# Kernel optimization log

Measured on AMD Instinct MI355X. Metric: run time of the kernel, lower is better.

The kernel has to match this reference:

```python
import jax, jax.numpy as jnp
import numpy as np

N = 50000
IN_CH = 128
HID = 64
HEADS = 4
OUT_CH = 2
E = 800000
NEG_SLOPE = 0.2


def setup_inputs() -> dict:
    key = jax.random.key(0)
    ks = jax.random.split(key, 10)
    x = jax.random.normal(ks[0], (N, IN_CH), dtype=jnp.float32)
    edge_index = jax.random.randint(ks[1], (2, E), 0, N, dtype=jnp.int64)
    # layer 1: GATConv(IN_CH -> HID, heads=HEADS, concat=True)
    s1 = 1.0 / np.sqrt(IN_CH)
    W1 = jax.random.normal(ks[2], (IN_CH, HEADS * HID), dtype=jnp.float32) * s1
    a_src1 = jax.random.normal(ks[3], (HEADS, HID), dtype=jnp.float32) * (1.0 / np.sqrt(HID))
    a_dst1 = jax.random.normal(ks[4], (HEADS, HID), dtype=jnp.float32) * (1.0 / np.sqrt(HID))
    b1 = jnp.zeros((HEADS * HID,), dtype=jnp.float32)
    # layer 2: GATConv(HEADS*HID -> OUT_CH, heads=1, concat=False)
    s2 = 1.0 / np.sqrt(HEADS * HID)
    W2 = jax.random.normal(ks[5], (HEADS * HID, OUT_CH), dtype=jnp.float32) * s2
    a_src2 = jax.random.normal(ks[6], (1, OUT_CH), dtype=jnp.float32) * (1.0 / np.sqrt(OUT_CH))
    a_dst2 = jax.random.normal(ks[7], (1, OUT_CH), dtype=jnp.float32) * (1.0 / np.sqrt(OUT_CH))
    b2 = jnp.zeros((OUT_CH,), dtype=jnp.float32)
    return {"x": x, "edge_index": edge_index, "W1": W1, "a_src1": a_src1,
            "a_dst1": a_dst1, "b1": b1, "W2": W2, "a_src2": a_src2,
            "a_dst2": a_dst2, "b2": b2}


def gat_conv(x, W, a_src, a_dst, bias, src, dst, heads, ch, concat):
    n = x.shape[0]
    h = (x @ W).reshape(n, heads, ch)                       # [N,H,C]
    al_s = jnp.sum(h * a_src[None], axis=-1)                # [N,H]
    al_d = jnp.sum(h * a_dst[None], axis=-1)                # [N,H]
    e = al_s[src] + al_d[dst]                               # [E,H]
    e = jnp.where(e > 0, e, NEG_SLOPE * e)                  # leaky_relu
    # segment softmax over edges grouped by destination node
    m = jax.ops.segment_max(e, dst, num_segments=n)         # [N,H]
    m = jnp.where(jnp.isfinite(m), m, 0.0)
    p = jnp.exp(e - m[dst])                                 # [E,H]
    denom = jax.ops.segment_sum(p, dst, num_segments=n)     # [N,H]
    alpha = p / (denom[dst] + 1e-16)                        # [E,H]
    msg = h[src] * alpha[:, :, None]                        # [E,H,C]
    out = jax.ops.segment_sum(msg, dst, num_segments=n)     # [N,H,C]
    if concat:
        out = out.reshape(n, heads * ch) + bias
    else:
        out = out.mean(axis=1) + bias
    return out


def reference(x, edge_index, W1, a_src1, a_dst1, b1, W2, a_src2, a_dst2, b2):
    n = x.shape[0]
    # PyG GATConv default: add self-loops
    loops = jnp.arange(n, dtype=edge_index.dtype)
    src = jnp.concatenate([edge_index[0], loops])
    dst = jnp.concatenate([edge_index[1], loops])
    h = gat_conv(x, W1, a_src1, a_dst1, b1, src, dst, HEADS, HID, True)
    h = jax.nn.relu(h)
    out = gat_conv(h, W2, a_src2, a_dst2, b2, src, dst, 1, OUT_CH, False)
    return out
```

## Files before the change

kernel.cpp:

```cpp
#include <hip/hip_runtime.h>

#define NNODE 50000
#define NEDGE 800000
#define NTOT  (NEDGE + NNODE)
#define NB_SCAN 49
#define NGEMM 1564

typedef __attribute__((ext_vector_type(8))) short bf16x8;
typedef __attribute__((ext_vector_type(4))) float f32x4;
union U4B8 { uint4 u; bf16x8 b; };

__device__ __forceinline__ unsigned short f2bf(float f) {
  union { float f; unsigned u; } v; v.f = f;
  unsigned r = v.u + 0x7FFFu + ((v.u >> 16) & 1u);
  return (unsigned short)(r >> 16);
}
__device__ __forceinline__ float bflo(unsigned u) {
  union { unsigned u; float f; } v; v.u = u << 16; return v.f;
}
__device__ __forceinline__ float bfhi(unsigned u) {
  union { unsigned u; float f; } v; v.u = u & 0xFFFF0000u; return v.f;
}
__device__ __forceinline__ unsigned packbf(float a, float b) {
  return (unsigned)f2bf(a) | ((unsigned)f2bf(b) << 16);
}

__global__ __launch_bounds__(256) void k_prep(const float* __restrict__ W1,
                                              unsigned short* __restrict__ W1bT,
                                              int* __restrict__ deg) {
  const int b = (int)blockIdx.x;
  if (b < 32) {
    int flat = b * 256 + threadIdx.x;
    int k = flat >> 6, c4 = (flat & 63) << 2;
    float4 v = *(const float4*)(W1 + k * 256 + c4);
    W1bT[(c4 + 0) * 128 + k] = f2bf(v.x);
    W1bT[(c4 + 1) * 128 + k] = f2bf(v.y);
    W1bT[(c4 + 2) * 128 + k] = f2bf(v.z);
    W1bT[(c4 + 3) * 128 + k] = f2bf(v.w);
  } else {
    int i = (b - 32) * 256 + threadIdx.x;
    if (i < NNODE) deg[i] = 0;
  }
}

__global__ __launch_bounds__(256) void k_gemm_deg(
    const float* __restrict__ x, const unsigned short* __restrict__ W1bT,
    const float* __restrict__ a_s1, const float* __restrict__ a_d1,
    unsigned short* __restrict__ h1b, float* __restrict__ als1,
    float* __restrict__ ald1, const int* __restrict__ ei,
    int* __restrict__ deg) {
  __shared__ unsigned short xs[64 * 136];
  if ((int)blockIdx.x >= NGEMM) {
    int i = ((int)blockIdx.x - NGEMM) * 256 + threadIdx.x;
    if (i < NTOT) {
      int d = (i < NEDGE) ? ei[NEDGE + i] : (i - NEDGE);
      atomicAdd(deg + d, 1);
    }
    return;
  }
  const int t = threadIdx.x;
  const int rb = (int)blockIdx.x >> 1, nhalf = (int)blockIdx.x & 1;
  const int grow0 = rb * 64;
#pragma unroll
  for (int i = 0; i < 8; ++i) {
    int f = t + i * 256;
    int row = f >> 5, c4 = (f & 31) << 2;
    int gr = grow0 + row;
    float4 v = make_float4(0.f, 0.f, 0.f, 0.f);
    if (gr < NNODE) v = *(const float4*)(x + gr * 128 + c4);
    *(uint2*)(xs + row * 136 + c4) = make_uint2(packbf(v.x, v.y), packbf(v.z, v.w));
  }
  const int wid = t >> 6, lane = t & 63;
  const int wrow = (wid >> 1) * 32;
  const int head = nhalf * 2 + (wid & 1);
  const int c_lo = lane & 15, g = lane >> 4;
  U4B8 bfr[4][4];
#pragma unroll
  for (int nr = 0; nr < 4; ++nr) {
    int c = head * 64 + nr * 16 + c_lo;
#pragma unroll
    for (int ks = 0; ks < 4; ++ks)
      bfr[nr][ks].u = *(const uint4*)(W1bT + c * 128 + ks * 32 + g * 8);
  }
  __syncthreads();
  U4B8 afr[2][4];
#pragma unroll
  for (int mr = 0; mr < 2; ++mr)
#pragma unroll
    for (int ks = 0; ks < 4; ++ks)
      afr[mr][ks].u = *(const uint4*)(xs + (wrow + mr * 16 + c_lo) * 136 + ks * 32 + g * 8);
  f32x4 acc[2][4];
#pragma unroll
  for (int mr = 0; mr < 2; ++mr)
#pragma unroll
    for (int nr = 0; nr < 4; ++nr) acc[mr][nr] = (f32x4){0.f, 0.f, 0.f, 0.f};
#pragma unroll
  for (int ks = 0; ks < 4; ++ks)
#pragma unroll
    for (int mr = 0; mr < 2; ++mr)
#pragma unroll
      for (int nr = 0; nr < 4; ++nr)
        acc[mr][nr] = __builtin_amdgcn_mfma_f32_16x16x32_bf16(
            afr[mr][ks].b, bfr[nr][ks].b, acc[mr][nr], 0, 0, 0);
  float as_v[4], ad_v[4];
#pragma unroll
  for (int nr = 0; nr < 4; ++nr) {
    as_v[nr] = a_s1[head * 64 + nr * 16 + c_lo];
    ad_v[nr] = a_d1[head * 64 + nr * 16 + c_lo];
  }
  float ps[2][4], pd[2][4];
#pragma unroll
  for (int mr = 0; mr < 2; ++mr)
#pragma unroll
    for (int r = 0; r < 4; ++r) {
      float s = 0.f, dsum = 0.f;
#pragma unroll
      for (int nr = 0; nr < 4; ++nr) {
        s += acc[mr][nr][r] * as_v[nr];
        dsum += acc[mr][nr][r] * ad_v[nr];
      }
      ps[mr][r] = s; pd[mr][r] = dsum;
    }
#pragma unroll
  for (int m = 1; m < 16; m <<= 1)
#pragma unroll
    for (int mr = 0; mr < 2; ++mr)
#pragma unroll
      for (int r = 0; r < 4; ++r) {
        ps[mr][r] += __shfl_xor(ps[mr][r], m, 64);
        pd[mr][r] += __shfl_xor(pd[mr][r], m, 64);
      }
  if (c_lo == 0) {
#pragma unroll
    for (int mr = 0; mr < 2; ++mr)
#pragma unroll
      for (int r = 0; r < 4; ++r) {
        int node = grow0 + wrow + mr * 16 + g * 4 + r;
        if (node < NNODE) {
          als1[node * 4 + head] = ps[mr][r];
          ald1[node * 4 + head] = pd[mr][r];
        }
      }
  }
  __syncthreads();
  unsigned short* tb = xs + wid * 2048;
#pragma unroll
  for (int mr = 0; mr < 2; ++mr)
#pragma unroll
    for (int nr = 0; nr < 4; ++nr)
#pragma unroll
      for (int r = 0; r < 4; ++r)
        tb[(mr * 16 + g * 4 + r) * 64 + nr * 16 + c_lo] = f2bf(acc[mr][nr][r]);
#pragma unroll
  for (int i = 0; i < 4; ++i) {
    int unit = i * 64 + lane;
    int row = unit >> 3, cS = (unit & 7) * 8;
    int node = grow0 + wrow + row;
    if (node < NNODE) {
      uint4 v = *(const uint4*)(tb + unit * 8);
      *(uint4*)(h1b + (size_t)node * 256 + nhalf * 128 + (wid & 1) * 64 + cS) = v;
    }
  }
}

__global__ __launch_bounds__(1024) void k_scan1(const int* __restrict__ deg,
                                                int* __restrict__ rowptr,
                                                int* __restrict__ bsum) {
  __shared__ int sh[1024];
  const int t = threadIdx.x;
  const int idx = (int)blockIdx.x * 1024 + t;
  int v = (idx < NNODE) ? deg[idx] : 0;
  sh[t] = v;
  __syncthreads();
#pragma unroll
  for (int off = 1; off < 1024; off <<= 1) {
    int add = (t >= off) ? sh[t - off] : 0;
    __syncthreads();
    sh[t] += add;
    __syncthreads();
  }
  if (idx < NNODE) rowptr[idx + 1] = sh[t];
  if (t == 1023) bsum[blockIdx.x] = sh[1023];
}

__global__ __launch_bounds__(256) void k_scan23(const int* __restrict__ deg,
                                                int* __restrict__ rowptr,
                                                const int* __restrict__ bsum,
                                                int* __restrict__ cursor) {
  __shared__ int boff[64];
  const int t = threadIdx.x;
  if (t < 64) {
    int v = (t < NB_SCAN) ? bsum[t] : 0;
    int orig = v;
#pragma unroll
    for (int off = 1; off < 64; off <<= 1) {
      int n = __shfl_up(v, off, 64);
      if (t >= off) v += n;
    }
    boff[t] = v - orig;
  }
  __syncthreads();
  int idx = (int)blockIdx.x * 256 + t;
  if (idx < NNODE) {
    int incl = rowptr[idx + 1] + boff[idx >> 10];
    rowptr[idx + 1] = incl;
    cursor[idx] = incl - deg[idx];
    if (idx == 0) rowptr[0] = 0;
  }
}

__global__ void k_scatter(const int* __restrict__ ei, int* __restrict__ cursor,
                          int* __restrict__ esrc) {
  int i = (int)blockIdx.x * blockDim.x + threadIdx.x;
  if (i >= NTOT) return;
  int s, d;
  if (i < NEDGE) { s = ei[i]; d = ei[NEDGE + i]; }
  else           { s = i - NEDGE; d = s; }
  int pos = atomicAdd(cursor + d, 1);
  esrc[pos] = s;
}

__global__ __launch_bounds__(256) void k_agg1(
    const unsigned short* __restrict__ h1b, const float* __restrict__ als1,
    const float* __restrict__ ald1, const int* __restrict__ rowptr,
    const int* __restrict__ esrc, const float* __restrict__ b1,
    const float* __restrict__ W2, const float* __restrict__ a_s2,
    const float* __restrict__ a_d2, float4* __restrict__ h2c) {
  const int w = threadIdx.x >> 6, lane = threadIdx.x & 63;
  const int d = (int)blockIdx.x * 4 + w;
  const int half = lane >> 5, cl = lane & 31;
  const int head = cl >> 3;
  const float ald = ald1[d * 4 + head];
  const int begin = rowptr[d], end = rowptr[d + 1];
  float acc[8];
#pragma unroll
  for (int i = 0; i < 8; ++i) acc[i] = 0.f;
  float S = 0.f;

  int j = begin + half;
  int s = (j < end) ? esrc[j] : -1;
  while (s >= 0) {
    const uint4 hv = *(const uint4*)(h1b + (size_t)s * 256 + cl * 8);
    float e = als1[s * 4 + head] + ald;
    int jn = j + 2;
    int sn = (jn < end) ? esrc[jn] : -1;
    e = fmaxf(e, 0.2f * e);
    float wgt = __expf(e);
    S += wgt;
    acc[0] += wgt * bflo(hv.x); acc[1] += wgt * bfhi(hv.x);
    acc[2] += wgt * bflo(hv.y); acc[3] += wgt * bfhi(hv.y);
    acc[4] += wgt * bflo(hv.z); acc[5] += wgt * bfhi(hv.z);
    acc[6] += wgt * bflo(hv.w); acc[7] += wgt * bfhi(hv.w);
    j = jn; s = sn;
  }
  S += __shfl_xor(S, 32, 64);
#pragma unroll
  for (int i = 0; i < 8; ++i) acc[i] += __shfl_xor(acc[i], 32, 64);

  const float inv = 1.f / S;
  const int c0 = cl * 8;
  float4 ba = *(const float4*)(b1 + c0);
  float4 bb = *(const float4*)(b1 + c0 + 4);
  float bias[8] = {ba.x, ba.y, ba.z, ba.w, bb.x, bb.y, bb.z, bb.w};
  float4 w0 = *(const float4*)(W2 + c0 * 2);
  float4 w1 = *(const float4*)(W2 + c0 * 2 + 4);
  float4 w2 = *(const float4*)(W2 + c0 * 2 + 8);
  float4 w3 = *(const float4*)(W2 + c0 * 2 + 12);
  float wa[16] = {w0.x, w0.y, w0.z, w0.w, w1.x, w1.y, w1.z, w1.w,
                  w2.x, w2.y, w2.z, w2.w, w3.x, w3.y, w3.z, w3.w};
  float p0 = 0.f, p1 = 0.f;
#pragma unroll
  for (int i = 0; i < 8; ++i) {
    float v = acc[i] * inv + bias[i];
    v = v > 0.f ? v : 0.f;
    p0 += v * wa[2 * i];
    p1 += v * wa[2 * i + 1];
  }
#pragma unroll
  for (int m = 1; m < 32; m <<= 1) {
    p0 += __shfl_xor(p0, m, 64);
    p1 += __shfl_xor(p1, m, 64);
  }
  if (lane == 0) {
    h2c[d] = make_float4(p0, p1,
                         p0 * a_s2[0] + p1 * a_s2[1],
                         p0 * a_d2[0] + p1 * a_d2[1]);
  }
}

__global__ __launch_bounds__(256) void k_agg2(
    const float4* __restrict__ h2c, const int* __restrict__ rowptr,
    const int* __restrict__ esrc, const float* __restrict__ b2,
    float* __restrict__ out) {
  int d = (int)blockIdx.x * 256 + threadIdx.x;
  if (d >= NNODE) return;
  const float ald = h2c[d].w;
  const int begin = rowptr[d], end = rowptr[d + 1];
  float S = 0.f, a0 = 0.f, a1 = 0.f;
  for (int j = begin; j < end; ++j) {
    int s = esrc[j];
    float4 v = h2c[s];
    float e = v.z + ald;
    e = fmaxf(e, 0.2f * e);
    float wgt = __expf(e);
    S += wgt;
    a0 += wgt * v.x;
    a1 += wgt * v.y;
  }
  float inv = 1.f / S;
  out[d * 2 + 0] = a0 * inv + b2[0];
  out[d * 2 + 1] = a1 * inv + b2[1];
}

static inline size_t algn(size_t x) { return (x + 255) & ~(size_t)255; }

extern "C" void kernel_launch(void* const* d_in, const int* in_sizes, int n_in,
                              void* d_out, int out_size, void* d_ws, size_t ws_size,
                              hipStream_t stream) {
  const float* x    = (const float*)d_in[0];
  const int*   ei   = (const int*)d_in[1];
  const float* W1   = (const float*)d_in[2];
  const float* a_s1 = (const float*)d_in[3];
  const float* a_d1 = (const float*)d_in[4];
  const float* b1   = (const float*)d_in[5];
  const float* W2   = (const float*)d_in[6];
  const float* a_s2 = (const float*)d_in[7];
  const float* a_d2 = (const float*)d_in[8];
  const float* b2   = (const float*)d_in[9];
  float* out = (float*)d_out;

  char* w = (char*)d_ws;
  size_t o = 0;
  unsigned short* h1b = (unsigned short*)(w + o); o += algn((size_t)NNODE * 256 * 2);
  unsigned short* W1bT = (unsigned short*)(w + o); o += algn((size_t)256 * 128 * 2);
  float* als1 = (float*)(w + o); o += algn((size_t)NNODE * 4 * 4);
  float* ald1 = (float*)(w + o); o += algn((size_t)NNODE * 4 * 4);
  int*   deg  = (int*)(w + o);   o += algn((size_t)NNODE * 4);
  int*   rowp = (int*)(w + o);   o += algn((size_t)(NNODE + 1) * 4);
  int*   curs = (int*)(w + o);   o += algn((size_t)NNODE * 4);
  int*   esrc = (int*)(w + o);   o += algn((size_t)NTOT * 4);
  int*   bsum = (int*)(w + o);   o += 256;
  float4* h2c = (float4*)(w + o); o += algn((size_t)NNODE * 16);
  (void)ws_size; (void)n_in; (void)in_sizes; (void)out_size;

  k_prep<<<dim3(32 + 196), dim3(256), 0, stream>>>(W1, W1bT, deg);
  k_gemm_deg<<<dim3(NGEMM + (NTOT + 255) / 256), dim3(256), 0, stream>>>(
      x, W1bT, a_s1, a_d1, h1b, als1, ald1, ei, deg);
  k_scan1<<<dim3(NB_SCAN), dim3(1024), 0, stream>>>(deg, rowp, bsum);
  k_scan23<<<dim3((NNODE + 255) / 256), dim3(256), 0, stream>>>(deg, rowp, bsum, curs);
  k_scatter<<<dim3((NTOT + 255) / 256), dim3(256), 0, stream>>>(ei, curs, esrc);
  k_agg1<<<dim3(12500), dim3(256), 0, stream>>>(h1b, als1, ald1, rowp, esrc, b1,
                                                W2, a_s2, a_d2, h2c);
  k_agg2<<<dim3((NNODE + 255) / 256), dim3(256), 0, stream>>>(h2c, rowp, esrc, b2, out);
}
```

Before: 262.7 us.

## Record edge rank during degree count and widen agg1 edge parallelism

```diff
diff --git a/kernel.cpp b/kernel.cpp
--- a/kernel.cpp
+++ b/kernel.cpp
@@ -48,13 +48,13 @@
     const float* __restrict__ a_s1, const float* __restrict__ a_d1,
     unsigned short* __restrict__ h1b, float* __restrict__ als1,
     float* __restrict__ ald1, const int* __restrict__ ei,
-    int* __restrict__ deg) {
+    int* __restrict__ deg, int* __restrict__ rank) {
   __shared__ unsigned short xs[64 * 136];
   if ((int)blockIdx.x >= NGEMM) {
     int i = ((int)blockIdx.x - NGEMM) * 256 + threadIdx.x;
     if (i < NTOT) {
       int d = (i < NEDGE) ? ei[NEDGE + i] : (i - NEDGE);
-      atomicAdd(deg + d, 1);
+      rank[i] = atomicAdd(deg + d, 1);
     }
     return;
   }
@@ -183,10 +183,8 @@
   if (t == 1023) bsum[blockIdx.x] = sh[1023];
 }
 
-__global__ __launch_bounds__(256) void k_scan23(const int* __restrict__ deg,
-                                                int* __restrict__ rowptr,
-                                                const int* __restrict__ bsum,
-                                                int* __restrict__ cursor) {
+__global__ __launch_bounds__(256) void k_scan23(int* __restrict__ rowptr,
+                                                const int* __restrict__ bsum) {
   __shared__ int boff[64];
   const int t = threadIdx.x;
   if (t < 64) {
@@ -202,22 +200,21 @@
   __syncthreads();
   int idx = (int)blockIdx.x * 256 + t;
   if (idx < NNODE) {
-    int incl = rowptr[idx + 1] + boff[idx >> 10];
-    rowptr[idx + 1] = incl;
-    cursor[idx] = incl - deg[idx];
+    rowptr[idx + 1] += boff[idx >> 10];
     if (idx == 0) rowptr[0] = 0;
   }
 }
 
-__global__ void k_scatter(const int* __restrict__ ei, int* __restrict__ cursor,
+__global__ void k_scatter(const int* __restrict__ ei,
+                          const int* __restrict__ rowptr,
+                          const int* __restrict__ rank,
                           int* __restrict__ esrc) {
   int i = (int)blockIdx.x * blockDim.x + threadIdx.x;
   if (i >= NTOT) return;
   int s, d;
   if (i < NEDGE) { s = ei[i]; d = ei[NEDGE + i]; }
   else           { s = i - NEDGE; d = s; }
-  int pos = atomicAdd(cursor + d, 1);
-  esrc[pos] = s;
+  esrc[rowptr[d] + rank[i]] = s;
 }
 
 __global__ __launch_bounds__(256) void k_agg1(
@@ -228,56 +225,67 @@
     const float* __restrict__ a_d2, float4* __restrict__ h2c) {
   const int w = threadIdx.x >> 6, lane = threadIdx.x & 63;
   const int d = (int)blockIdx.x * 4 + w;
-  const int half = lane >> 5, cl = lane & 31;
-  const int head = cl >> 3;
+  const int q = lane >> 4, cl = lane & 15;
+  const int head = cl >> 2;
   const float ald = ald1[d * 4 + head];
   const int begin = rowptr[d], end = rowptr[d + 1];
-  float acc[8];
-#pragma unroll
-  for (int i = 0; i < 8; ++i) acc[i] = 0.f;
+  float acc[16];
+#pragma unroll
+  for (int i = 0; i < 16; ++i) acc[i] = 0.f;
   float S = 0.f;
 
-  int j = begin + half;
-  int s = (j < end) ? esrc[j] : -1;
-  while (s >= 0) {
-    const uint4 hv = *(const uint4*)(h1b + (size_t)s * 256 + cl * 8);
+  for (int j = begin + q; j < end; j += 4) {
+    int s = esrc[j];
+    const unsigned short* hp = h1b + (size_t)s * 256 + cl * 16;
+    const uint4 hv0 = *(const uint4*)(hp);
+    const uint4 hv1 = *(const uint4*)(hp + 8);
     float e = als1[s * 4 + head] + ald;
-    int jn = j + 2;
-    int sn = (jn < end) ? esrc[jn] : -1;
     e = fmaxf(e, 0.2f * e);
     float wgt = __expf(e);
     S += wgt;
-    acc[0] += wgt * bflo(hv.x); acc[1] += wgt * bfhi(hv.x);
-    acc[2] += wgt * bflo(hv.y); acc[3] += wgt * bfhi(hv.y);
-    acc[4] += wgt * bflo(hv.z); acc[5] += wgt * bfhi(hv.z);
-    acc[6] += wgt * bflo(hv.w); acc[7] += wgt * bfhi(hv.w);
-    j = jn; s = sn;
-  }
+    acc[0]  += wgt * bflo(hv0.x); acc[1]  += wgt * bfhi(hv0.x);
+    acc[2]  += wgt * bflo(hv0.y); acc[3]  += wgt * bfhi(hv0.y);
+    acc[4]  += wgt * bflo(hv0.z); acc[5]  += wgt * bfhi(hv0.z);
+    acc[6]  += wgt * bflo(hv0.w); acc[7]  += wgt * bfhi(hv0.w);
+    acc[8]  += wgt * bflo(hv1.x); acc[9]  += wgt * bfhi(hv1.x);
+    acc[10] += wgt * bflo(hv1.y); acc[11] += wgt * bfhi(hv1.y);
+    acc[12] += wgt * bflo(hv1.z); acc[13] += wgt * bfhi(hv1.z);
+    acc[14] += wgt * bflo(hv1.w); acc[15] += wgt * bfhi(hv1.w);
+  }
+  S += __shfl_xor(S, 16, 64);
   S += __shfl_xor(S, 32, 64);
 #pragma unroll
-  for (int i = 0; i < 8; ++i) acc[i] += __shfl_xor(acc[i], 32, 64);
+  for (int i = 0; i < 16; ++i) {
+    acc[i] += __shfl_xor(acc[i], 16, 64);
+    acc[i] += __shfl_xor(acc[i], 32, 64);
+  }
 
   const float inv = 1.f / S;
-  const int c0 = cl * 8;
-  float4 ba = *(const float4*)(b1 + c0);
-  float4 bb = *(const float4*)(b1 + c0 + 4);
-  float bias[8] = {ba.x, ba.y, ba.z, ba.w, bb.x, bb.y, bb.z, bb.w};
-  float4 w0 = *(const float4*)(W2 + c0 * 2);
-  float4 w1 = *(const float4*)(W2 + c0 * 2 + 4);
-  float4 w2 = *(const float4*)(W2 + c0 * 2 + 8);
-  float4 w3 = *(const float4*)(W2 + c0 * 2 + 12);
-  float wa[16] = {w0.x, w0.y, w0.z, w0.w, w1.x, w1.y, w1.z, w1.w,
-                  w2.x, w2.y, w2.z, w2.w, w3.x, w3.y, w3.z, w3.w};
+  const int c0 = cl * 16;
+  float bias[16];
+#pragma unroll
+  for (int i = 0; i < 4; ++i) {
+    float4 bv = *(const float4*)(b1 + c0 + i * 4);
+    bias[4 * i] = bv.x; bias[4 * i + 1] = bv.y;
+    bias[4 * i + 2] = bv.z; bias[4 * i + 3] = bv.w;
+  }
+  float wa[32];
+#pragma unroll
+  for (int i = 0; i < 8; ++i) {
+    float4 wv = *(const float4*)(W2 + c0 * 2 + i * 4);
+    wa[4 * i] = wv.x; wa[4 * i + 1] = wv.y;
+    wa[4 * i + 2] = wv.z; wa[4 * i + 3] = wv.w;
+  }
   float p0 = 0.f, p1 = 0.f;
 #pragma unroll
-  for (int i = 0; i < 8; ++i) {
+  for (int i = 0; i < 16; ++i) {
     float v = acc[i] * inv + bias[i];
     v = v > 0.f ? v : 0.f;
     p0 += v * wa[2 * i];
     p1 += v * wa[2 * i + 1];
   }
 #pragma unroll
-  for (int m = 1; m < 32; m <<= 1) {
+  for (int m = 1; m < 16; m <<= 1) {
     p0 += __shfl_xor(p0, m, 64);
     p1 += __shfl_xor(p1, m, 64);
   }
@@ -337,7 +345,7 @@
   float* ald1 = (float*)(w + o); o += algn((size_t)NNODE * 4 * 4);
   int*   deg  = (int*)(w + o);   o += algn((size_t)NNODE * 4);
   int*   rowp = (int*)(w + o);   o += algn((size_t)(NNODE + 1) * 4);
-  int*   curs = (int*)(w + o);   o += algn((size_t)NNODE * 4);
+  int*   rank = (int*)(w + o);   o += algn((size_t)NTOT * 4);
   int*   esrc = (int*)(w + o);   o += algn((size_t)NTOT * 4);
   int*   bsum = (int*)(w + o);   o += 256;
   float4* h2c = (float4*)(w + o); o += algn((size_t)NNODE * 16);
@@ -345,10 +353,10 @@
 
   k_prep<<<dim3(32 + 196), dim3(256), 0, stream>>>(W1, W1bT, deg);
   k_gemm_deg<<<dim3(NGEMM + (NTOT + 255) / 256), dim3(256), 0, stream>>>(
-      x, W1bT, a_s1, a_d1, h1b, als1, ald1, ei, deg);
+      x, W1bT, a_s1, a_d1, h1b, als1, ald1, ei, deg, rank);
   k_scan1<<<dim3(NB_SCAN), dim3(1024), 0, stream>>>(deg, rowp, bsum);
-  k_scan23<<<dim3((NNODE + 255) / 256), dim3(256), 0, stream>>>(deg, rowp, bsum, curs);
-  k_scatter<<<dim3((NTOT + 255) / 256), dim3(256), 0, stream>>>(ei, curs, esrc);
+  k_scan23<<<dim3((NNODE + 255) / 256), dim3(256), 0, stream>>>(rowp, bsum);
+  k_scatter<<<dim3((NTOT + 255) / 256), dim3(256), 0, stream>>>(ei, rowp, rank, esrc);
   k_agg1<<<dim3(12500), dim3(256), 0, stream>>>(h1b, als1, ald1, rowp, esrc, b1,
                                                 W2, a_s2, a_d2, h2c);
   k_agg2<<<dim3((NNODE + 255) / 256), dim3(256), 0, stream>>>(h2c, rowp, esrc, b2, out);
```

Result: faster. 251.0 us (-4.5%).

## Record per-edge atomic rank during degree count and fuse scan finalize with scatter

Applied to the files above, without the earlier changes.

```diff
diff --git a/kernel.cpp b/kernel.cpp
--- a/kernel.cpp
+++ b/kernel.cpp
@@ -48,13 +48,13 @@
     const float* __restrict__ a_s1, const float* __restrict__ a_d1,
     unsigned short* __restrict__ h1b, float* __restrict__ als1,
     float* __restrict__ ald1, const int* __restrict__ ei,
-    int* __restrict__ deg) {
+    int* __restrict__ deg, int* __restrict__ rank) {
   __shared__ unsigned short xs[64 * 136];
   if ((int)blockIdx.x >= NGEMM) {
     int i = ((int)blockIdx.x - NGEMM) * 256 + threadIdx.x;
     if (i < NTOT) {
       int d = (i < NEDGE) ? ei[NEDGE + i] : (i - NEDGE);
-      atomicAdd(deg + d, 1);
+      rank[i] = atomicAdd(deg + d, 1);
     }
     return;
   }
@@ -164,7 +164,7 @@
 }
 
 __global__ __launch_bounds__(1024) void k_scan1(const int* __restrict__ deg,
-                                                int* __restrict__ rowptr,
+                                                int* __restrict__ rowp,
                                                 int* __restrict__ bsum) {
   __shared__ int sh[1024];
   const int t = threadIdx.x;
@@ -179,14 +179,14 @@
     sh[t] += add;
     __syncthreads();
   }
-  if (idx < NNODE) rowptr[idx + 1] = sh[t];
+  if (idx < NNODE) rowp[idx + 1] = sh[t];
   if (t == 1023) bsum[blockIdx.x] = sh[1023];
 }
 
-__global__ __launch_bounds__(256) void k_scan23(const int* __restrict__ deg,
-                                                int* __restrict__ rowptr,
-                                                const int* __restrict__ bsum,
-                                                int* __restrict__ cursor) {
+__global__ __launch_bounds__(256) void k_scanscatter(
+    const int* __restrict__ ei, const int* __restrict__ rowp,
+    const int* __restrict__ bsum, const int* __restrict__ rank,
+    int* __restrict__ rowf, int* __restrict__ esrc) {
   __shared__ int boff[64];
   const int t = threadIdx.x;
   if (t < 64) {
@@ -200,24 +200,18 @@
     boff[t] = v - orig;
   }
   __syncthreads();
-  int idx = (int)blockIdx.x * 256 + t;
-  if (idx < NNODE) {
-    int incl = rowptr[idx + 1] + boff[idx >> 10];
-    rowptr[idx + 1] = incl;
-    cursor[idx] = incl - deg[idx];
-    if (idx == 0) rowptr[0] = 0;
-  }
-}
-
-__global__ void k_scatter(const int* __restrict__ ei, int* __restrict__ cursor,
-                          int* __restrict__ esrc) {
-  int i = (int)blockIdx.x * blockDim.x + threadIdx.x;
-  if (i >= NTOT) return;
-  int s, d;
-  if (i < NEDGE) { s = ei[i]; d = ei[NEDGE + i]; }
-  else           { s = i - NEDGE; d = s; }
-  int pos = atomicAdd(cursor + d, 1);
-  esrc[pos] = s;
+  const int i = (int)blockIdx.x * 256 + t;
+  if (i < NNODE) {
+    rowf[i + 1] = rowp[i + 1] + boff[i >> 10];
+    if (i == 0) rowf[0] = 0;
+  }
+  if (i < NTOT) {
+    int s, d;
+    if (i < NEDGE) { s = ei[i]; d = ei[NEDGE + i]; }
+    else           { s = i - NEDGE; d = s; }
+    int base = (d == 0) ? 0 : rowp[d] + boff[(d - 1) >> 10];
+    esrc[base + rank[i]] = s;
+  }
 }
 
 __global__ __launch_bounds__(256) void k_agg1(
@@ -337,7 +331,8 @@
   float* ald1 = (float*)(w + o); o += algn((size_t)NNODE * 4 * 4);
   int*   deg  = (int*)(w + o);   o += algn((size_t)NNODE * 4);
   int*   rowp = (int*)(w + o);   o += algn((size_t)(NNODE + 1) * 4);
-  int*   curs = (int*)(w + o);   o += algn((size_t)NNODE * 4);
+  int*   rowf = (int*)(w + o);   o += algn((size_t)(NNODE + 1) * 4);
+  int*   rank = (int*)(w + o);   o += algn((size_t)NTOT * 4);
   int*   esrc = (int*)(w + o);   o += algn((size_t)NTOT * 4);
   int*   bsum = (int*)(w + o);   o += 256;
   float4* h2c = (float4*)(w + o); o += algn((size_t)NNODE * 16);
@@ -345,11 +340,11 @@
 
   k_prep<<<dim3(32 + 196), dim3(256), 0, stream>>>(W1, W1bT, deg);
   k_gemm_deg<<<dim3(NGEMM + (NTOT + 255) / 256), dim3(256), 0, stream>>>(
-      x, W1bT, a_s1, a_d1, h1b, als1, ald1, ei, deg);
+      x, W1bT, a_s1, a_d1, h1b, als1, ald1, ei, deg, rank);
   k_scan1<<<dim3(NB_SCAN), dim3(1024), 0, stream>>>(deg, rowp, bsum);
-  k_scan23<<<dim3((NNODE + 255) / 256), dim3(256), 0, stream>>>(deg, rowp, bsum, curs);
-  k_scatter<<<dim3((NTOT + 255) / 256), dim3(256), 0, stream>>>(ei, curs, esrc);
-  k_agg1<<<dim3(12500), dim3(256), 0, stream>>>(h1b, als1, ald1, rowp, esrc, b1,
+  k_scanscatter<<<dim3((NTOT + 255) / 256), dim3(256), 0, stream>>>(
+      ei, rowp, bsum, rank, rowf, esrc);
+  k_agg1<<<dim3(12500), dim3(256), 0, stream>>>(h1b, als1, ald1, rowf, esrc, b1,
                                                 W2, a_s2, a_d2, h2c);
-  k_agg2<<<dim3((NNODE + 255) / 256), dim3(256), 0, stream>>>(h2c, rowp, esrc, b2, out);
-}
+  k_agg2<<<dim3((NNODE + 255) / 256), dim3(256), 0, stream>>>(h2c, rowf, esrc, b2, out);
+}
```

After: 227.9 us. -13.3%, faster.
